# Kernel tuning notes

Measured on AMD Instinct MI355X. Metric: run time of the kernel, lower is better.

The kernel has to match this reference:

```python
import jax, jax.numpy as jnp
import numpy as np
from jax import lax

STRIDE = 2  # down_sample_stride
MATMUL_NORM = True


def maxpool2d_5d(x, s):
    # x: [B, T, C, H, W]; kernel=s, stride=s, padding=(s-1)//2 == 0 for s=2
    return lax.reduce_window(
        x, -jnp.inf, lax.max,
        window_dimensions=(1, 1, 1, s, s),
        window_strides=(1, 1, 1, s, s),
        padding='VALID')


def setup_inputs() -> dict:
    key = jax.random.key(0)
    k1, k2, k3, k4 = jax.random.split(key, 4)
    B, T, Ck, Cv, H, W = 2, 4, 64, 256, 64, 64
    return {
        'memory_keys': jax.random.normal(k1, (B, T, Ck, H, W), jnp.float32),
        'memory_values': jax.random.normal(k2, (B, T, Cv, H, W), jnp.float32),
        'query_key': jax.random.normal(k3, (B, Ck, H, W), jnp.float32),
        'query_value': jax.random.normal(k4, (B, Cv, H, W), jnp.float32),
    }


def reference(memory_keys, memory_values, query_key, query_value):
    B, T, Ck, oH, oW = memory_keys.shape
    Cv = memory_values.shape[2]
    # down-sample memory bank (max pool, stride 2, no padding)
    mk = maxpool2d_5d(memory_keys, STRIDE)   # [B,T,Ck,h,w]
    mv = maxpool2d_5d(memory_values, STRIDE) # [B,T,Cv,h,w]
    h, w = mk.shape[-2], mk.shape[-1]
    M = T * h * w
    N = oH * oH  # code uses ori_height*ori_height (square assumed)
    # permute(0,2,1,3,4).view(B,Ck,M).permute(0,2,1) -> [B, M, Ck]
    mk = mk.transpose(0, 2, 1, 3, 4).reshape(B, Ck, M).transpose(0, 2, 1)
    qk = query_key.reshape(B, Ck, N)
    attn = jnp.einsum('bmc,bcn->bmn', mk, qk)  # [B, M, N]
    if MATMUL_NORM:
        attn = attn * (Ck ** -0.5)
    attn = jax.nn.softmax(attn, axis=1)  # softmax over memory positions
    mv = mv.transpose(0, 2, 1, 3, 4).reshape(B, Cv, M)
    memory = jnp.einsum('bcm,bmn->bcn', mv, attn).reshape(B, Cv, oH, oW)
    return jnp.concatenate([query_value, memory], axis=1)  # [B, 2*Cv, H, W]
```

## Files before the change

kernel.cpp:

```cpp
#include <hip/hip_runtime.h>
#include <hip/hip_bf16.h>

typedef unsigned short u16;
typedef unsigned int   u32;
typedef __attribute__((ext_vector_type(8))) short  bf16x8;
typedef __attribute__((ext_vector_type(4))) float  floatx4;

#define NB 2
#define NT 4
#define CK 64
#define CV 256
#define HH 64
#define WW 64
#define MM 4096
#define NN 4096
#define SCALE 0.125f
#define SHIFT 4.0f
#define OUT_B 2097152
#define NW 64
#define NIT 32

__device__ __forceinline__ u16 f2b(float f) {
    __hip_bfloat16 h = __float2bfloat16(f);
    union { __hip_bfloat16 h; u16 u; } v; v.h = h; return v.u;
}

#define PRE_K 65536
#define PRE_V 589824
#define PRE_T 1114112

__global__ void prep(const float* __restrict__ mk, const float* __restrict__ mv,
                     const float4* __restrict__ qv,
                     u16* __restrict__ pk2, u16* __restrict__ vt,
                     float* __restrict__ out) {
    int u = blockIdx.x * 256 + threadIdx.x;
    if (u < PRE_K) {
        int m = u & 4095, cb8 = (u >> 12) & 7, b = u >> 15;
        int t = m >> 10, hh = (m >> 5) & 31, ww = m & 31;
        const float* s0 = mk + ((size_t)((b*NT + t)*CK + cb8*8))*(HH*WW)
                             + (2*hh)*WW + 2*ww;
        bf16x8 fr;
        #pragma unroll
        for (int i = 0; i < 8; ++i) {
            const float* s = s0 + (size_t)i*(HH*WW);
            float2 r0 = *(const float2*)s;
            float2 r1 = *(const float2*)(s + WW);
            fr[i] = (short)f2b(fmaxf(fmaxf(r0.x, r0.y), fmaxf(r1.x, r1.y)));
        }
        *(bf16x8*)(pk2 + ((size_t)(b*8 + cb8)*MM + m)*8) = fr;
    } else if (u < PRE_V) {
        int u2 = u - PRE_K;
        int m4 = u2 & 1023, c = (u2 >> 10) & 255, b = u2 >> 18;
        int t = m4 >> 8, hh = (m4 >> 3) & 31, w8 = m4 & 7;
        const float* s0 = mv + ((size_t)((b*NT + t)*CV + c))*(HH*WW)
                             + (2*hh)*WW + 8*w8;
        float4 a0 = *(const float4*)(s0);
        float4 a1 = *(const float4*)(s0 + 4);
        float4 b0 = *(const float4*)(s0 + WW);
        float4 b1 = *(const float4*)(s0 + WW + 4);
        ushort4 r;
        r.x = f2b(fmaxf(fmaxf(a0.x, a0.y), fmaxf(b0.x, b0.y)));
        r.y = f2b(fmaxf(fmaxf(a0.z, a0.w), fmaxf(b0.z, b0.w)));
        r.z = f2b(fmaxf(fmaxf(a1.x, a1.y), fmaxf(b1.x, b1.y)));
        r.w = f2b(fmaxf(fmaxf(a1.z, a1.w), fmaxf(b1.z, b1.w)));
        *(ushort4*)(vt + ((size_t)(b*CV + c)*MM) + m4*4) = r;
    } else {
        int u3 = u - PRE_V;
        int b = u3 >> 18, ru = u3 & 262143;
        ((float4*)out)[(size_t)b*(OUT_B/4) + ru] = qv[u3];
    }
}

__device__ __forceinline__ void qk_phase(bf16x8 k0, bf16x8 k1,
        const bf16x8 (&qf)[2][4], float (&sacc)[4],
        u16* __restrict__ Pd, int lrow, int cbw, int sw)
{
    #pragma unroll
    for (int t = 0; t < 4; ++t) {
        floatx4 s = __builtin_amdgcn_mfma_f32_16x16x32_bf16(
                        k0, qf[0][t], (floatx4){0.f,0.f,0.f,0.f}, 0, 0, 0);
        s = __builtin_amdgcn_mfma_f32_16x16x32_bf16(k1, qf[1][t], s, 0, 0, 0);
        float p0 = __expf(s[0]*SCALE - SHIFT);
        float p1 = __expf(s[1]*SCALE - SHIFT);
        float p2 = __expf(s[2]*SCALE - SHIFT);
        float p3 = __expf(s[3]*SCALE - SHIFT);
        sacc[t] += (p0 + p1) + (p2 + p3);
        u32 d0 = (u32)f2b(p0) | ((u32)f2b(p1) << 16);
        u32 d1 = (u32)f2b(p2) | ((u32)f2b(p3) << 16);
        *(uint2*)&Pd[(t*16 + lrow)*128 + ((cbw ^ sw) << 2)] = make_uint2(d0, d1);
    }
}

__device__ __forceinline__ void pv_phase(const bf16x8 (&vf)[4],
        floatx4 (&oacc)[4], const u16* __restrict__ Ps,
        int lrow, int quad, int sw)
{
    #pragma unroll
    for (int cc = 0; cc < 4; ++cc) {
        bf16x8 pf[4];
        #pragma unroll
        for (int t = 0; t < 4; ++t) {
            int cb = (cc << 3) + (quad << 1);
            pf[t] = *(const bf16x8*)&Ps[(t*16 + lrow)*128 + ((cb ^ sw) << 2)];
        }
        __builtin_amdgcn_s_setprio(1);
        #pragma unroll
        for (int t = 0; t < 4; ++t)
            oacc[t] = __builtin_amdgcn_mfma_f32_16x16x32_bf16(
                          vf[cc], pf[t], oacc[t], 0, 0, 0);
        __builtin_amdgcn_s_setprio(0);
    }
}

__launch_bounds__(512, 2)
__global__ void attn_v3(const u16* __restrict__ pk2, const u16* __restrict__ vt,
                        const float* __restrict__ qk, float* __restrict__ out) {
    const int bid = blockIdx.x;
    const int xcd = bid & 7, grp = bid >> 3;
    const int b   = xcd >> 2, cs = (xcd >> 1) & 1;
    const int ntile = (xcd & 1) * 32 + grp;
    const int tid = threadIdx.x, w = tid >> 6, l = tid & 63;
    const int lrow = l & 15, quad = l >> 4;
    const int n0 = ntile * NW;
    const int sw  = lrow << 1;
    const int cbw = (w << 2) + quad;

    __shared__ u16  P[2][NW * 128];
    __shared__ float sums_s[8][NW];

    bf16x8 qf[2][4];
    const float* qb = qk + (size_t)b * CK * NN + n0;
    #pragma unroll
    for (int cc = 0; cc < 2; ++cc)
        #pragma unroll
        for (int t = 0; t < 4; ++t)
            #pragma unroll
            for (int i = 0; i < 8; ++i) {
                int c = cc*32 + quad*8 + i;
                qf[cc][t][i] = (short)f2b(qb[(size_t)c*NN + t*16 + lrow]);
            }

    const u16* pkb  = pk2 + (size_t)b * (8*MM*8);
    const int  mrw  = w*16 + lrow;
    const u16* vrow = vt + ((size_t)b*CV + cs*128 + w*16 + lrow)*MM + quad*8;

    floatx4 oacc[4];
    #pragma unroll
    for (int t = 0; t < 4; ++t) oacc[t] = (floatx4){0.f, 0.f, 0.f, 0.f};
    float sacc[4] = {0.f, 0.f, 0.f, 0.f};

    bf16x8 k0 = *(const bf16x8*)(pkb + ((size_t)quad*MM + mrw)*8);
    bf16x8 k1 = *(const bf16x8*)(pkb + ((size_t)(quad+4)*MM + mrw)*8);
    bf16x8 vf[4];
    #pragma unroll
    for (int cc = 0; cc < 4; ++cc)
        vf[cc] = *(const bf16x8*)(vrow + cc*32);
    qk_phase(k0, k1, qf, sacc, P[0], lrow, cbw, sw);

    for (int it = 0; it < NIT - 1; ++it) {
        __syncthreads();
        const int mb2 = (it + 1) << 7;
        bf16x8 k0n = *(const bf16x8*)(pkb + ((size_t)quad*MM + mb2 + mrw)*8);
        bf16x8 k1n = *(const bf16x8*)(pkb + ((size_t)(quad+4)*MM + mb2 + mrw)*8);
        bf16x8 vn[4];
        #pragma unroll
        for (int cc = 0; cc < 4; ++cc)
            vn[cc] = *(const bf16x8*)(vrow + mb2 + cc*32);
        pv_phase(vf, oacc, P[it & 1], lrow, quad, sw);
        qk_phase(k0n, k1n, qf, sacc, P[(it + 1) & 1], lrow, cbw, sw);
        #pragma unroll
        for (int cc = 0; cc < 4; ++cc) vf[cc] = vn[cc];
    }
    __syncthreads();
    pv_phase(vf, oacc, P[(NIT - 1) & 1], lrow, quad, sw);

    #pragma unroll
    for (int t = 0; t < 4; ++t) {
        float v = sacc[t];
        v += __shfl_xor(v, 16, 64);
        v += __shfl_xor(v, 32, 64);
        if (l < 16) sums_s[w][t*16 + l] = v;
    }
    __syncthreads();
    float inv[4];
    #pragma unroll
    for (int t = 0; t < 4; ++t) {
        float d = 0.f;
        #pragma unroll
        for (int w2 = 0; w2 < 8; ++w2) d += sums_s[w2][t*16 + lrow];
        inv[t] = 1.0f / d;
    }

    float* ob = out + ((size_t)(b*512 + 256 + cs*128))*NN + n0;
    #pragma unroll
    for (int t = 0; t < 4; ++t)
        #pragma unroll
        for (int r = 0; r < 4; ++r) {
            int c_loc = w*16 + quad*4 + r;
            ob[(size_t)c_loc*NN + t*16 + lrow] = oacc[t][r] * inv[t];
        }
}


__global__ void pool_v_f32(const float* __restrict__ src, float* __restrict__ out) {
    int e = blockIdx.x * 256 + threadIdx.x;
    int c = e & 255;
    int r = e >> 8;
    int ww = r & 31;  int hh = (r >> 5) & 31;
    int t  = (r >> 10) & 3;  int b = r >> 12;
    int m  = r & (MM - 1);
    const float* s = src + ((size_t)(((b*NT + t)*CV + c)*HH + 2*hh))*WW + 2*ww;
    out[(size_t)b*OUT_B + (size_t)m*CV + c] = fmaxf(fmaxf(s[0], s[1]), fmaxf(s[WW], s[WW+1]));
}

__global__ void pool_k_f32(const float* __restrict__ src, float* __restrict__ dst) {
    int e = blockIdx.x * 256 + threadIdx.x;
    int c = e & 63;
    int r = e >> 6;
    int ww = r & 31;  int hh = (r >> 5) & 31;
    int t  = (r >> 10) & 3;  int b = r >> 12;
    const float* s = src + ((size_t)(((b*NT + t)*CK + c)*HH + 2*hh))*WW + 2*ww;
    dst[e] = fmaxf(fmaxf(s[0], s[1]), fmaxf(s[WW], s[WW+1]));
}

__global__ void copy_qv_f32(const float4* __restrict__ src, float4* __restrict__ dst) {
    int u = blockIdx.x * 256 + threadIdx.x;
    int b  = u >> 18;
    int ru = u & 262143;
    dst[(size_t)b * (OUT_B/4) + ru] = src[u];
}

template<bool STAGED_K>
__launch_bounds__(256)
__global__ void attn_old(const float* __restrict__ pk,
                         const float* __restrict__ mk,
                         const float* __restrict__ qk,
                         float* __restrict__ out) {
    __shared__ __align__(16) float q_lds[CK][4];
    __shared__ __align__(16) float sarr[4][MM];
    __shared__ float inv_l[4];

    const int tid = threadIdx.x;
    const int blk = blockIdx.x;
    const int b   = blk >> 10;
    const int n0  = (blk & 1023) << 2;

    {
        int c = tid >> 2, qi = tid & 3;
        q_lds[c][qi] = qk[((size_t)(b*CK + c))*NN + n0 + qi];
    }
    __syncthreads();

    #pragma unroll
    for (int i = 0; i < 16; ++i) {
        int m = tid + (i << 8);
        float a0 = 0.f, a1 = 0.f, a2 = 0.f, a3 = 0.f;
        if (STAGED_K) {
            const float4* k4 = reinterpret_cast<const float4*>(pk + ((size_t)b*MM + m)*CK);
            #pragma unroll
            for (int cc = 0; cc < 16; ++cc) {
                float4 kv = k4[cc];
                int c = cc*4;
                float4 q0 = *reinterpret_cast<const float4*>(&q_lds[c][0]);
                float4 q1 = *reinterpret_cast<const float4*>(&q_lds[c+1][0]);
                float4 q2 = *reinterpret_cast<const float4*>(&q_lds[c+2][0]);
                float4 q3 = *reinterpret_cast<const float4*>(&q_lds[c+3][0]);
                a0 += kv.x*q0.x + kv.y*q1.x + kv.z*q2.x + kv.w*q3.x;
                a1 += kv.x*q0.y + kv.y*q1.y + kv.z*q2.y + kv.w*q3.y;
                a2 += kv.x*q0.z + kv.y*q1.z + kv.z*q2.z + kv.w*q3.z;
                a3 += kv.x*q0.w + kv.y*q1.w + kv.z*q2.w + kv.w*q3.w;
            }
        } else {
            int ww = m & 31, hh = (m >> 5) & 31, t = m >> 10;
            const float* base = mk + ((size_t)((b*NT + t)*CK)*HH + 2*hh)*WW + 2*ww;
            for (int c = 0; c < CK; ++c) {
                const float* s = base + (size_t)c*HH*WW;
                float kv = fmaxf(fmaxf(s[0], s[1]), fmaxf(s[WW], s[WW+1]));
                float4 q = *reinterpret_cast<const float4*>(&q_lds[c][0]);
                a0 += kv*q.x; a1 += kv*q.y; a2 += kv*q.z; a3 += kv*q.w;
            }
        }
        sarr[0][m] = a0*SCALE;
        sarr[1][m] = a1*SCALE;
        sarr[2][m] = a2*SCALE;
        sarr[3][m] = a3*SCALE;
    }
    __syncthreads();

    const int wave = tid >> 6, lane = tid & 63;
    float mx = -3.0e38f;
    for (int m = lane; m < MM; m += 64) mx = fmaxf(mx, sarr[wave][m]);
    #pragma unroll
    for (int off = 32; off > 0; off >>= 1) mx = fmaxf(mx, __shfl_xor(mx, off, 64));
    float ls = 0.f;
    for (int m = lane; m < MM; m += 64) {
        float p = __expf(sarr[wave][m] - mx);
        sarr[wave][m] = p;
        ls += p;
    }
    #pragma unroll
    for (int off = 32; off > 0; off >>= 1) ls += __shfl_xor(ls, off, 64);
    if (lane == 0) inv_l[wave] = 1.0f / ls;
    __syncthreads();

    const int c4 = lane;
    const float4* vb = reinterpret_cast<const float4*>(out + (size_t)b*OUT_B) + c4;
    const float* prow = sarr[wave];
    float a0 = 0.f, a1 = 0.f, a2 = 0.f, a3 = 0.f;
    for (int m = 0; m < MM; m += 4) {
        float4 p4 = *reinterpret_cast<const float4*>(prow + m);
        const float4* vp = vb + (size_t)m*(CV/4);
        float4 v0 = vp[0], v1 = vp[CV/4], v2 = vp[CV/2], v3 = vp[3*(CV/4)];
        a0 += p4.x*v0.x + p4.y*v1.x + p4.z*v2.x + p4.w*v3.x;
        a1 += p4.x*v0.y + p4.y*v1.y + p4.z*v2.y + p4.w*v3.y;
        a2 += p4.x*v0.z + p4.y*v1.z + p4.z*v2.z + p4.w*v3.z;
        a3 += p4.x*v0.w + p4.y*v1.w + p4.z*v2.w + p4.w*v3.w;
    }

    float inv = inv_l[wave];
    int n = n0 + wave;
    size_t ob = ((size_t)(b*512 + 256 + c4*4))*NN + n;
    out[ob]        = a0*inv;
    out[ob + NN]   = a1*inv;
    out[ob + 2*NN] = a2*inv;
    out[ob + 3*NN] = a3*inv;
}


extern "C" void kernel_launch(void* const* d_in, const int* in_sizes, int n_in,
                              void* d_out, int out_size, void* d_ws, size_t ws_size,
                              hipStream_t stream) {
    const float* mk = (const float*)d_in[0];
    const float* mv = (const float*)d_in[1];
    const float* qk = (const float*)d_in[2];
    const float* qv = (const float*)d_in[3];
    float* out = (float*)d_out;

    u16* pk2 = (u16*)d_ws;
    u16* vt  = pk2 + (size_t)NB*8*MM*8;
    const size_t need = ((size_t)NB*8*MM*8 + (size_t)NB*CV*MM) * sizeof(u16);

    if (ws_size >= need) {
        prep<<<PRE_T/256, 256, 0, stream>>>(mk, mv, (const float4*)qv, pk2, vt, out);
        attn_v3<<<256, 512, 0, stream>>>(pk2, vt, qk, out);
    } else {
        const size_t pk_bytes = (size_t)NB*MM*CK*sizeof(float);
        const bool staged = (ws_size >= pk_bytes);
        float* pk = (float*)d_ws;
        pool_v_f32<<<(NB*MM*CV)/256, 256, 0, stream>>>(mv, out);
        if (staged) {
            pool_k_f32<<<(NB*MM*CK)/256, 256, 0, stream>>>(mk, pk);
            attn_old<true ><<<NB*(NN/4), 256, 0, stream>>>(pk, mk, qk, out);
        } else {
            attn_old<false><<<NB*(NN/4), 256, 0, stream>>>(pk, mk, qk, out);
        }
        copy_qv_f32<<<((NB*CV*HH*WW)/4)/256, 256, 0, stream>>>((const float4*)qv, (float4*)out);
    }
}
```

Measured before the change: 143.7 us.

## Split memory dimension across two wave groups per block and merge partial outputs

Doubles the block to 1024 threads, with two 512-thread groups each covering half of the memory positions (split-K over M). Each group keeps its own double-buffered P tile in shared memory. The partial outputs are combined through shared memory before normalization and the store. Occupancy per CU rises and each block's serial loop is half as long, at the cost of an extra reduction pass, more LDS, and tighter register limits from launch_bounds(1024,4). The exponent is also rewritten as exp2 of a single FMA with prefolded constants.

```diff
diff --git a/kernel.cpp b/kernel.cpp
--- a/kernel.cpp
+++ b/kernel.cpp
@@ -1,5 +1,6 @@
 #include <hip/hip_runtime.h>
 #include <hip/hip_bf16.h>
+#include <math.h>
 
 typedef unsigned short u16;
 typedef unsigned int   u32;
@@ -18,7 +19,9 @@
 #define SHIFT 4.0f
 #define OUT_B 2097152
 #define NW 64
-#define NIT 32
+#define ITG 16
+#define C1 0.18033688011112042f
+#define C2 (-5.770780163555853f)
 
 __device__ __forceinline__ u16 f2b(float f) {
     __hip_bfloat16 h = __float2bfloat16(f);
@@ -80,10 +83,10 @@
         floatx4 s = __builtin_amdgcn_mfma_f32_16x16x32_bf16(
                         k0, qf[0][t], (floatx4){0.f,0.f,0.f,0.f}, 0, 0, 0);
         s = __builtin_amdgcn_mfma_f32_16x16x32_bf16(k1, qf[1][t], s, 0, 0, 0);
-        float p0 = __expf(s[0]*SCALE - SHIFT);
-        float p1 = __expf(s[1]*SCALE - SHIFT);
-        float p2 = __expf(s[2]*SCALE - SHIFT);
-        float p3 = __expf(s[3]*SCALE - SHIFT);
+        float p0 = exp2f(__builtin_fmaf(s[0], C1, C2));
+        float p1 = exp2f(__builtin_fmaf(s[1], C1, C2));
+        float p2 = exp2f(__builtin_fmaf(s[2], C1, C2));
+        float p3 = exp2f(__builtin_fmaf(s[3], C1, C2));
         sacc[t] += (p0 + p1) + (p2 + p3);
         u32 d0 = (u32)f2b(p0) | ((u32)f2b(p1) << 16);
         u32 d1 = (u32)f2b(p2) | ((u32)f2b(p3) << 16);
@@ -112,21 +115,24 @@
     }
 }
 
-__launch_bounds__(512, 2)
-__global__ void attn_v3(const u16* __restrict__ pk2, const u16* __restrict__ vt,
+__launch_bounds__(1024, 4)
+__global__ void attn_v4(const u16* __restrict__ pk2, const u16* __restrict__ vt,
                         const float* __restrict__ qk, float* __restrict__ out) {
     const int bid = blockIdx.x;
     const int xcd = bid & 7, grp = bid >> 3;
     const int b   = xcd >> 2, cs = (xcd >> 1) & 1;
     const int ntile = (xcd & 1) * 32 + grp;
-    const int tid = threadIdx.x, w = tid >> 6, l = tid & 63;
+    const int tid = threadIdx.x;
+    const int wg  = tid >> 9;
+    const int w   = (tid >> 6) & 7, l = tid & 63;
     const int lrow = l & 15, quad = l >> 4;
     const int n0 = ntile * NW;
     const int sw  = lrow << 1;
     const int cbw = (w << 2) + quad;
-
-    __shared__ u16  P[2][NW * 128];
-    __shared__ float sums_s[8][NW];
+    const int mstart = wg << 11;
+
+    __shared__ __align__(16) u16 P[2][2][NW * 128];
+    __shared__ float sums_s[16][NW];
 
     bf16x8 qf[2][4];
     const float* qb = qk + (size_t)b * CK * NN + n0;
@@ -141,8 +147,9 @@
             }
 
     const u16* pkb  = pk2 + (size_t)b * (8*MM*8);
-    const int  mrw  = w*16 + lrow;
-    const u16* vrow = vt + ((size_t)b*CV + cs*128 + w*16 + lrow)*MM + quad*8;
+    const int  mrw  = mstart + w*16 + lrow;
+    const u16* vrow = vt + ((size_t)b*CV + cs*128 + w*16 + lrow)*MM
+                         + mstart + quad*8;
 
     floatx4 oacc[4];
     #pragma unroll
@@ -155,9 +162,9 @@
     #pragma unroll
     for (int cc = 0; cc < 4; ++cc)
         vf[cc] = *(const bf16x8*)(vrow + cc*32);
-    qk_phase(k0, k1, qf, sacc, P[0], lrow, cbw, sw);
-
-    for (int it = 0; it < NIT - 1; ++it) {
+    qk_phase(k0, k1, qf, sacc, P[wg][0], lrow, cbw, sw);
+
+    for (int it = 0; it < ITG - 1; ++it) {
         __syncthreads();
         const int mb2 = (it + 1) << 7;
         bf16x8 k0n = *(const bf16x8*)(pkb + ((size_t)quad*MM + mb2 + mrw)*8);
@@ -166,39 +173,51 @@
         #pragma unroll
         for (int cc = 0; cc < 4; ++cc)
             vn[cc] = *(const bf16x8*)(vrow + mb2 + cc*32);
-        pv_phase(vf, oacc, P[it & 1], lrow, quad, sw);
-        qk_phase(k0n, k1n, qf, sacc, P[(it + 1) & 1], lrow, cbw, sw);
+        pv_phase(vf, oacc, P[wg][it & 1], lrow, quad, sw);
+        qk_phase(k0n, k1n, qf, sacc, P[wg][(it + 1) & 1], lrow, cbw, sw);
         #pragma unroll
         for (int cc = 0; cc < 4; ++cc) vf[cc] = vn[cc];
     }
     __syncthreads();
-    pv_phase(vf, oacc, P[(NIT - 1) & 1], lrow, quad, sw);
+    pv_phase(vf, oacc, P[wg][(ITG - 1) & 1], lrow, quad, sw);
 
     #pragma unroll
     for (int t = 0; t < 4; ++t) {
         float v = sacc[t];
         v += __shfl_xor(v, 16, 64);
         v += __shfl_xor(v, 32, 64);
-        if (l < 16) sums_s[w][t*16 + l] = v;
-    }
-    __syncthreads();
-    float inv[4];
-    #pragma unroll
-    for (int t = 0; t < 4; ++t) {
-        float d = 0.f;
-        #pragma unroll
-        for (int w2 = 0; w2 < 8; ++w2) d += sums_s[w2][t*16 + lrow];
-        inv[t] = 1.0f / d;
-    }
-
-    float* ob = out + ((size_t)(b*512 + 256 + cs*128))*NN + n0;
-    #pragma unroll
-    for (int t = 0; t < 4; ++t)
-        #pragma unroll
-        for (int r = 0; r < 4; ++r) {
-            int c_loc = w*16 + quad*4 + r;
-            ob[(size_t)c_loc*NN + t*16 + lrow] = oacc[t][r] * inv[t];
-        }
+        if (l < 16) sums_s[wg*8 + w][t*16 + l] = v;
+    }
+    __syncthreads();
+
+    float* cbuf = (float*)&P[0][0][0];
+    if (wg == 1) {
+        #pragma unroll
+        for (int t = 0; t < 4; ++t)
+            #pragma unroll
+            for (int r = 0; r < 4; ++r)
+                cbuf[(t*4 + r)*512 + w*64 + l] = oacc[t][r];
+    }
+    __syncthreads();
+    if (wg == 0) {
+        float inv[4];
+        #pragma unroll
+        for (int t = 0; t < 4; ++t) {
+            float d = 0.f;
+            #pragma unroll
+            for (int w2 = 0; w2 < 16; ++w2) d += sums_s[w2][t*16 + lrow];
+            inv[t] = 1.0f / d;
+        }
+        float* ob = out + ((size_t)(b*512 + 256 + cs*128))*NN + n0;
+        #pragma unroll
+        for (int t = 0; t < 4; ++t)
+            #pragma unroll
+            for (int r = 0; r < 4; ++r) {
+                int c_loc = w*16 + quad*4 + r;
+                float v = oacc[t][r] + cbuf[(t*4 + r)*512 + w*64 + l];
+                ob[(size_t)c_loc*NN + t*16 + lrow] = v * inv[t];
+            }
+    }
 }
 
 
@@ -342,7 +361,7 @@
 
     if (ws_size >= need) {
         prep<<<PRE_T/256, 256, 0, stream>>>(mk, mv, (const float4*)qv, pk2, vt, out);
-        attn_v3<<<256, 512, 0, stream>>>(pk2, vt, qk, out);
+        attn_v4<<<256, 1024, 0, stream>>>(pk2, vt, qk, out);
     } else {
         const size_t pk_bytes = (size_t)NB*MM*CK*sizeof(float);
         const bool staged = (ws_size >= pk_bytes);
```

New measurement: 149.5 us. +4.0%, slower.

## Stage K/V tiles into LDS via async global_load_lds with double buffering

Applied to the files above, without the earlier changes.

Replaces direct register loads of K and V fragments from global memory with asynchronous global-to-LDS copies (global_load_lds). The copies are issued two iterations ahead into double-buffered swizzled LDS tiles and gated by vmcnt waits, so load latency should overlap the MFMA work. The exp is also folded into a single fma plus exp2. This raises LDS usage, which may limit the two-blocks-per-CU occupancy, and adds explicit waitcnt and scheduling barriers that must remain correct.

```diff
diff --git a/kernel.cpp b/kernel.cpp
--- a/kernel.cpp
+++ b/kernel.cpp
@@ -1,5 +1,6 @@
 #include <hip/hip_runtime.h>
 #include <hip/hip_bf16.h>
+#include <math.h>
 
 typedef unsigned short u16;
 typedef unsigned int   u32;
@@ -19,10 +20,19 @@
 #define OUT_B 2097152
 #define NW 64
 #define NIT 32
+#define C1 0.18033688011112042f
+#define C2 (-5.770780163555853f)
+
+#define AS1 __attribute__((address_space(1)))
+#define AS3 __attribute__((address_space(3)))
 
 __device__ __forceinline__ u16 f2b(float f) {
     __hip_bfloat16 h = __float2bfloat16(f);
     union { __hip_bfloat16 h; u16 u; } v; v.h = h; return v.u;
+}
+
+__device__ __forceinline__ void gload16(const void* g, void* l) {
+    __builtin_amdgcn_global_load_lds((const AS1 u32*)g, (AS3 u32*)l, 16, 0, 0);
 }
 
 #define PRE_K 65536
@@ -80,10 +90,10 @@
         floatx4 s = __builtin_amdgcn_mfma_f32_16x16x32_bf16(
                         k0, qf[0][t], (floatx4){0.f,0.f,0.f,0.f}, 0, 0, 0);
         s = __builtin_amdgcn_mfma_f32_16x16x32_bf16(k1, qf[1][t], s, 0, 0, 0);
-        float p0 = __expf(s[0]*SCALE - SHIFT);
-        float p1 = __expf(s[1]*SCALE - SHIFT);
-        float p2 = __expf(s[2]*SCALE - SHIFT);
-        float p3 = __expf(s[3]*SCALE - SHIFT);
+        float p0 = exp2f(__builtin_fmaf(s[0], C1, C2));
+        float p1 = exp2f(__builtin_fmaf(s[1], C1, C2));
+        float p2 = exp2f(__builtin_fmaf(s[2], C1, C2));
+        float p3 = exp2f(__builtin_fmaf(s[3], C1, C2));
         sacc[t] += (p0 + p1) + (p2 + p3);
         u32 d0 = (u32)f2b(p0) | ((u32)f2b(p1) << 16);
         u32 d1 = (u32)f2b(p2) | ((u32)f2b(p3) << 16);
@@ -113,7 +123,7 @@
 }
 
 __launch_bounds__(512, 2)
-__global__ void attn_v3(const u16* __restrict__ pk2, const u16* __restrict__ vt,
+__global__ void attn_v6(const u16* __restrict__ pk2, const u16* __restrict__ vt,
                         const float* __restrict__ qk, float* __restrict__ out) {
     const int bid = blockIdx.x;
     const int xcd = bid & 7, grp = bid >> 3;
@@ -125,7 +135,9 @@
     const int sw  = lrow << 1;
     const int cbw = (w << 2) + quad;
 
-    __shared__ u16  P[2][NW * 128];
+    __shared__ __align__(16) u16 P[2][NW * 128];
+    __shared__ __align__(16) u16 Kl[2][8][1024];
+    __shared__ __align__(16) u16 Vl[2][8][2048];
     __shared__ float sums_s[8][NW];
 
     bf16x8 qf[2][4];
@@ -140,39 +152,76 @@
                 qf[cc][t][i] = (short)f2b(qb[(size_t)c*NN + t*16 + lrow]);
             }
 
-    const u16* pkb  = pk2 + (size_t)b * (8*MM*8);
-    const int  mrw  = w*16 + lrow;
-    const u16* vrow = vt + ((size_t)b*CV + cs*128 + w*16 + lrow)*MM + quad*8;
+    const u16* pkb = pk2 + (size_t)b * (8*MM*8);
+    const u16* vtb = vt + ((size_t)b*CV + cs*128) * MM;
 
     floatx4 oacc[4];
     #pragma unroll
     for (int t = 0; t < 4; ++t) oacc[t] = (floatx4){0.f, 0.f, 0.f, 0.f};
     float sacc[4] = {0.f, 0.f, 0.f, 0.f};
 
-    bf16x8 k0 = *(const bf16x8*)(pkb + ((size_t)quad*MM + mrw)*8);
-    bf16x8 k1 = *(const bf16x8*)(pkb + ((size_t)(quad+4)*MM + mrw)*8);
-    bf16x8 vf[4];
-    #pragma unroll
-    for (int cc = 0; cc < 4; ++cc)
-        vf[cc] = *(const bf16x8*)(vrow + cc*32);
-    qk_phase(k0, k1, qf, sacc, P[0], lrow, cbw, sw);
+    #define STAGE(buf, mb)                                                     \
+        do {                                                                   \
+            _Pragma("unroll")                                                  \
+            for (int i_ = 0; i_ < 4; ++i_) {                                   \
+                int c_  = (l >> 4) + i_*4;                                     \
+                int mc_ = (l & 15) ^ c_;                                       \
+                gload16(vtb + (size_t)(w*16 + c_)*MM + (mb) + mc_*8,           \
+                        &Vl[buf][w][i_*512]);                                  \
+            }                                                                  \
+            _Pragma("unroll")                                                  \
+            for (int i_ = 0; i_ < 2; ++i_) {                                   \
+                int cb_ = (l >> 4) + i_*4;                                     \
+                gload16(pkb + ((size_t)cb_*MM + (mb) + w*16 + (l & 15))*8,     \
+                        &Kl[buf][w][i_*512]);                                  \
+            }                                                                  \
+        } while (0)
+
+    STAGE(0, 0);
+    STAGE(1, 128);
+    asm volatile("s_waitcnt vmcnt(6)" ::: "memory");
+    __builtin_amdgcn_sched_barrier(0);
+    {
+        const u16* Kw = &Kl[0][w][0];
+        bf16x8 k0 = *(const bf16x8*)&Kw[(size_t)l * 8];
+        bf16x8 k1 = *(const bf16x8*)&Kw[(size_t)(l + 64) * 8];
+        qk_phase(k0, k1, qf, sacc, P[0], lrow, cbw, sw);
+    }
 
     for (int it = 0; it < NIT - 1; ++it) {
         __syncthreads();
-        const int mb2 = (it + 1) << 7;
-        bf16x8 k0n = *(const bf16x8*)(pkb + ((size_t)quad*MM + mb2 + mrw)*8);
-        bf16x8 k1n = *(const bf16x8*)(pkb + ((size_t)(quad+4)*MM + mb2 + mrw)*8);
-        bf16x8 vn[4];
+        const int cur = it & 1, nxt = cur ^ 1;
+        {
+            const u16* Vw = &Vl[cur][w][0];
+            bf16x8 vf[4];
+            #pragma unroll
+            for (int cc = 0; cc < 4; ++cc)
+                vf[cc] = *(const bf16x8*)
+                         &Vw[(size_t)(lrow*16 + ((cc*4 + quad) ^ lrow)) * 8];
+            pv_phase(vf, oacc, P[cur], lrow, quad, sw);
+        }
+        int itn = it + 2; if (itn > NIT - 1) itn = NIT - 1;
+        STAGE(cur, itn << 7);
+        asm volatile("s_waitcnt vmcnt(6)" ::: "memory");
+        __builtin_amdgcn_sched_barrier(0);
+        {
+            const u16* Kw = &Kl[nxt][w][0];
+            bf16x8 k0 = *(const bf16x8*)&Kw[(size_t)l * 8];
+            bf16x8 k1 = *(const bf16x8*)&Kw[(size_t)(l + 64) * 8];
+            qk_phase(k0, k1, qf, sacc, P[nxt], lrow, cbw, sw);
+        }
+    }
+    __syncthreads();
+    {
+        const u16* Vw = &Vl[(NIT - 1) & 1][w][0];
+        bf16x8 vf[4];
         #pragma unroll
         for (int cc = 0; cc < 4; ++cc)
-            vn[cc] = *(const bf16x8*)(vrow + mb2 + cc*32);
-        pv_phase(vf, oacc, P[it & 1], lrow, quad, sw);
-        qk_phase(k0n, k1n, qf, sacc, P[(it + 1) & 1], lrow, cbw, sw);
-        #pragma unroll
-        for (int cc = 0; cc < 4; ++cc) vf[cc] = vn[cc];
-    }
-    __syncthreads();
-    pv_phase(vf, oacc, P[(NIT - 1) & 1], lrow, quad, sw);
+            vf[cc] = *(const bf16x8*)
+                     &Vw[(size_t)(lrow*16 + ((cc*4 + quad) ^ lrow)) * 8];
+        pv_phase(vf, oacc, P[(NIT - 1) & 1], lrow, quad, sw);
+    }
+    #undef STAGE
 
     #pragma unroll
     for (int t = 0; t < 4; ++t) {
@@ -342,7 +391,7 @@
 
     if (ws_size >= need) {
         prep<<<PRE_T/256, 256, 0, stream>>>(mk, mv, (const float4*)qv, pk2, vt, out);
-        attn_v3<<<256, 512, 0, stream>>>(pk2, vt, qk, out);
+        attn_v6<<<256, 512, 0, stream>>>(pk2, vt, qk, out);
     } else {
         const size_t pk_bytes = (size_t)NB*MM*CK*sizeof(float);
         const bool staged = (ws_size >= pk_bytes);
```

Result: slower. 148.3 us (+3.2%).

## Split Cv into quarters per block, doubling grid and halving PV accumulators

Applied to the files above, without the earlier changes.

The attention kernel now launches 512 blocks, each covering 64 value channels instead of 128. Each wave pair splits the 64 query columns in half, so every wave holds only two PV accumulators. The launch bound is raised to 4 blocks per SM to improve occupancy and latency hiding. The exp is rewritten as exp2 of a fused multiply-add with folded constants. The QK^T and exp work is now recomputed by twice as many blocks, which adds redundant compute.

```diff
diff --git a/kernel.cpp b/kernel.cpp
--- a/kernel.cpp
+++ b/kernel.cpp
@@ -1,5 +1,6 @@
 #include <hip/hip_runtime.h>
 #include <hip/hip_bf16.h>
+#include <math.h>
 
 typedef unsigned short u16;
 typedef unsigned int   u32;
@@ -19,6 +20,8 @@
 #define OUT_B 2097152
 #define NW 64
 #define NIT 32
+#define C1 0.18033688011112042f
+#define C2 (-5.770780163555853f)
 
 __device__ __forceinline__ u16 f2b(float f) {
     __hip_bfloat16 h = __float2bfloat16(f);
@@ -80,10 +83,10 @@
         floatx4 s = __builtin_amdgcn_mfma_f32_16x16x32_bf16(
                         k0, qf[0][t], (floatx4){0.f,0.f,0.f,0.f}, 0, 0, 0);
         s = __builtin_amdgcn_mfma_f32_16x16x32_bf16(k1, qf[1][t], s, 0, 0, 0);
-        float p0 = __expf(s[0]*SCALE - SHIFT);
-        float p1 = __expf(s[1]*SCALE - SHIFT);
-        float p2 = __expf(s[2]*SCALE - SHIFT);
-        float p3 = __expf(s[3]*SCALE - SHIFT);
+        float p0 = exp2f(__builtin_fmaf(s[0], C1, C2));
+        float p1 = exp2f(__builtin_fmaf(s[1], C1, C2));
+        float p2 = exp2f(__builtin_fmaf(s[2], C1, C2));
+        float p3 = exp2f(__builtin_fmaf(s[3], C1, C2));
         sacc[t] += (p0 + p1) + (p2 + p3);
         u32 d0 = (u32)f2b(p0) | ((u32)f2b(p1) << 16);
         u32 d1 = (u32)f2b(p2) | ((u32)f2b(p3) << 16);
@@ -92,40 +95,36 @@
 }
 
 __device__ __forceinline__ void pv_phase(const bf16x8 (&vf)[4],
-        floatx4 (&oacc)[4], const u16* __restrict__ Ps,
-        int lrow, int quad, int sw)
+        floatx4 (&oacc)[2], const u16* __restrict__ Ps,
+        int lrow, int quad, int sw, int ntw)
 {
     #pragma unroll
-    for (int cc = 0; cc < 4; ++cc) {
-        bf16x8 pf[4];
-        #pragma unroll
-        for (int t = 0; t < 4; ++t) {
-            int cb = (cc << 3) + (quad << 1);
-            pf[t] = *(const bf16x8*)&Ps[(t*16 + lrow)*128 + ((cb ^ sw) << 2)];
-        }
+    for (int s = 0; s < 4; ++s) {
+        int cb = (s << 3) + (quad << 1);
+        bf16x8 pf0 = *(const bf16x8*)&Ps[(ntw*32 + lrow)*128 + ((cb ^ sw) << 2)];
+        bf16x8 pf1 = *(const bf16x8*)&Ps[(ntw*32 + 16 + lrow)*128 + ((cb ^ sw) << 2)];
         __builtin_amdgcn_s_setprio(1);
-        #pragma unroll
-        for (int t = 0; t < 4; ++t)
-            oacc[t] = __builtin_amdgcn_mfma_f32_16x16x32_bf16(
-                          vf[cc], pf[t], oacc[t], 0, 0, 0);
+        oacc[0] = __builtin_amdgcn_mfma_f32_16x16x32_bf16(vf[s], pf0, oacc[0], 0, 0, 0);
+        oacc[1] = __builtin_amdgcn_mfma_f32_16x16x32_bf16(vf[s], pf1, oacc[1], 0, 0, 0);
         __builtin_amdgcn_s_setprio(0);
     }
 }
 
-__launch_bounds__(512, 2)
-__global__ void attn_v3(const u16* __restrict__ pk2, const u16* __restrict__ vt,
+__launch_bounds__(512, 4)
+__global__ void attn_v7(const u16* __restrict__ pk2, const u16* __restrict__ vt,
                         const float* __restrict__ qk, float* __restrict__ out) {
     const int bid = blockIdx.x;
-    const int xcd = bid & 7, grp = bid >> 3;
-    const int b   = xcd >> 2, cs = (xcd >> 1) & 1;
-    const int ntile = (xcd & 1) * 32 + grp;
+    const int xcd = bid & 7;
+    const int b   = xcd >> 2, cs = xcd & 3;
+    const int ntile = bid >> 3;
     const int tid = threadIdx.x, w = tid >> 6, l = tid & 63;
     const int lrow = l & 15, quad = l >> 4;
     const int n0 = ntile * NW;
     const int sw  = lrow << 1;
     const int cbw = (w << 2) + quad;
-
-    __shared__ u16  P[2][NW * 128];
+    const int cw  = w >> 1, ntw = w & 1;
+
+    __shared__ __align__(16) u16 P[2][NW * 128];
     __shared__ float sums_s[8][NW];
 
     bf16x8 qf[2][4];
@@ -142,19 +141,19 @@
 
     const u16* pkb  = pk2 + (size_t)b * (8*MM*8);
     const int  mrw  = w*16 + lrow;
-    const u16* vrow = vt + ((size_t)b*CV + cs*128 + w*16 + lrow)*MM + quad*8;
-
-    floatx4 oacc[4];
-    #pragma unroll
-    for (int t = 0; t < 4; ++t) oacc[t] = (floatx4){0.f, 0.f, 0.f, 0.f};
+    const u16* vrow = vt + ((size_t)b*CV + cs*64 + cw*16 + lrow)*MM + quad*8;
+
+    floatx4 oacc[2];
+    oacc[0] = (floatx4){0.f, 0.f, 0.f, 0.f};
+    oacc[1] = (floatx4){0.f, 0.f, 0.f, 0.f};
     float sacc[4] = {0.f, 0.f, 0.f, 0.f};
 
     bf16x8 k0 = *(const bf16x8*)(pkb + ((size_t)quad*MM + mrw)*8);
     bf16x8 k1 = *(const bf16x8*)(pkb + ((size_t)(quad+4)*MM + mrw)*8);
     bf16x8 vf[4];
     #pragma unroll
-    for (int cc = 0; cc < 4; ++cc)
-        vf[cc] = *(const bf16x8*)(vrow + cc*32);
+    for (int s = 0; s < 4; ++s)
+        vf[s] = *(const bf16x8*)(vrow + s*32);
     qk_phase(k0, k1, qf, sacc, P[0], lrow, cbw, sw);
 
     for (int it = 0; it < NIT - 1; ++it) {
@@ -164,15 +163,15 @@
         bf16x8 k1n = *(const bf16x8*)(pkb + ((size_t)(quad+4)*MM + mb2 + mrw)*8);
         bf16x8 vn[4];
         #pragma unroll
-        for (int cc = 0; cc < 4; ++cc)
-            vn[cc] = *(const bf16x8*)(vrow + mb2 + cc*32);
-        pv_phase(vf, oacc, P[it & 1], lrow, quad, sw);
+        for (int s = 0; s < 4; ++s)
+            vn[s] = *(const bf16x8*)(vrow + mb2 + s*32);
+        pv_phase(vf, oacc, P[it & 1], lrow, quad, sw, ntw);
         qk_phase(k0n, k1n, qf, sacc, P[(it + 1) & 1], lrow, cbw, sw);
         #pragma unroll
-        for (int cc = 0; cc < 4; ++cc) vf[cc] = vn[cc];
-    }
-    __syncthreads();
-    pv_phase(vf, oacc, P[(NIT - 1) & 1], lrow, quad, sw);
+        for (int s = 0; s < 4; ++s) vf[s] = vn[s];
+    }
+    __syncthreads();
+    pv_phase(vf, oacc, P[(NIT - 1) & 1], lrow, quad, sw, ntw);
 
     #pragma unroll
     for (int t = 0; t < 4; ++t) {
@@ -182,22 +181,22 @@
         if (l < 16) sums_s[w][t*16 + l] = v;
     }
     __syncthreads();
-    float inv[4];
-    #pragma unroll
-    for (int t = 0; t < 4; ++t) {
+    float inv2[2];
+    #pragma unroll
+    for (int t2 = 0; t2 < 2; ++t2) {
         float d = 0.f;
         #pragma unroll
-        for (int w2 = 0; w2 < 8; ++w2) d += sums_s[w2][t*16 + lrow];
-        inv[t] = 1.0f / d;
-    }
-
-    float* ob = out + ((size_t)(b*512 + 256 + cs*128))*NN + n0;
-    #pragma unroll
-    for (int t = 0; t < 4; ++t)
+        for (int w2 = 0; w2 < 8; ++w2) d += sums_s[w2][ntw*32 + t2*16 + lrow];
+        inv2[t2] = 1.0f / d;
+    }
+
+    float* ob = out + ((size_t)(b*512 + 256 + cs*64))*NN + n0 + ntw*32;
+    #pragma unroll
+    for (int t2 = 0; t2 < 2; ++t2)
         #pragma unroll
         for (int r = 0; r < 4; ++r) {
-            int c_loc = w*16 + quad*4 + r;
-            ob[(size_t)c_loc*NN + t*16 + lrow] = oacc[t][r] * inv[t];
+            int c_loc = cw*16 + quad*4 + r;
+            ob[(size_t)c_loc*NN + t2*16 + lrow] = oacc[t2][r] * inv2[t2];
         }
 }
 
@@ -342,7 +341,7 @@
 
     if (ws_size >= need) {
         prep<<<PRE_T/256, 256, 0, stream>>>(mk, mv, (const float4*)qv, pk2, vt, out);
-        attn_v3<<<256, 512, 0, stream>>>(pk2, vt, qk, out);
+        attn_v7<<<512, 512, 0, stream>>>(pk2, vt, qk, out);
     } else {
         const size_t pk_bytes = (size_t)NB*MM*CK*sizeof(float);
         const bool staged = (ws_size >= pk_bytes);
```

Measured after the change: 162.8 us. +13.3%, slower.
